# Optimization experiments

Hardware: AMD Instinct MI355X
Metric: run time of the kernel (lower is better)

The kernel has to match this reference:

```python
import jax, jax.numpy as jnp
import numpy as np

H = W = 2048
P = 50000  # number of peaks
BACKGROUND = 0.1


def setup_inputs() -> dict:
    key = jax.random.key(0)
    k1, k2, k3, k4 = jax.random.split(key, 4)
    # coordinate meshes, X varies along columns, Y along rows (as in np.meshgrid)
    X, Y = jnp.meshgrid(jnp.arange(W, dtype=jnp.float32), jnp.arange(H, dtype=jnp.float32))
    margin = 32.0
    pos_x = jax.random.uniform(k1, (P,), jnp.float32, margin, W - margin - 1)
    pos_y = jax.random.uniform(k2, (P,), jnp.float32, margin, H - margin - 1)
    height = jax.random.uniform(k3, (P,), jnp.float32, 0.5, 2.0)
    width = jax.random.uniform(k4, (P,), jnp.float32, 2.0, 4.0)
    return {"X": X, "Y": Y, "pos_x": pos_x, "pos_y": pos_y, "height": height, "width": width}


def _gaussian(x, y, pos_x, pos_y, height, width):
    # isotropic Gaussian peak (concrete model_fn)
    r2 = (x - pos_x) ** 2 + (y - pos_y) ** 2
    return height * jnp.exp(-r2 / (2.0 * width ** 2))


def reference(X, Y, pos_x, pos_y, height, width):
    # window size from max width (static shape choice, computed concretely)
    width_max = float(jnp.max(width))
    window_size = int(5 * width_max)
    if window_size % 2 == 0:
        window_size += 1
    half = window_size // 2

    wr = jnp.arange(-half, half + 1, dtype=jnp.int32)
    window_X, window_Y = jnp.meshgrid(wr, wr)  # (ws, ws)
    window_coords = jnp.stack([window_X.ravel(), window_Y.ravel()], axis=-1)  # (ws*ws, 2) as (x, y)

    x_idx = jnp.round(pos_x - X[0, 0]).astype(jnp.int32)
    y_idx = jnp.round(pos_y - Y[0, 0]).astype(jnp.int32)
    peak_coords = jnp.stack([x_idx, y_idx], axis=-1)  # (P, 2)
    global_coords = peak_coords[:, None, :] + window_coords[None, :, :]  # (P, ws*ws, 2)

    # evaluate peak centered at 0 on the local window: (P, ws, ws)
    local_peaks = _gaussian(
        window_X[None, :, :].astype(X.dtype),
        window_Y[None, :, :].astype(X.dtype),
        0.0, 0.0,
        height[:, None, None], width[:, None, None],
    )
    local_flat = local_peaks.reshape(pos_x.shape[0], -1)  # (P, ws*ws)

    total = jnp.zeros_like(X) + BACKGROUND
    total = total.at[global_coords[:, :, 1], global_coords[:, :, 0]].add(local_flat)
    return total
```

## Files before the change

### kernel.cpp

```cpp
#include <hip/hip_runtime.h>


#define IMG_W 2048
#define IMG_H 2048
#define CELL_SHIFT 4
#define CELLS_X 128
#define NCELL (CELLS_X * CELLS_X)
#define CAP 20
#define REG 64
#define CH 32
#define CH_PAD 40
#define CANDMAX 256

typedef _Float16 half8 __attribute__((ext_vector_type(8)));
typedef float floatx4 __attribute__((ext_vector_type(4)));

__global__ void k_bin(const float* __restrict__ px, const float* __restrict__ py,
                      const float* __restrict__ ht, const float* __restrict__ wd,
                      int P, int* __restrict__ counts, unsigned int* __restrict__ wmax,
                      float4* __restrict__ bins) {
    int i = blockIdx.x * blockDim.x + threadIdx.x;
    bool live = (i < P);
    float w = live ? wd[i] : 0.0f;
    float wr = w;
    for (int m = 32; m >= 1; m >>= 1)
        wr = fmaxf(wr, __shfl_xor(wr, m));
    if ((threadIdx.x & 63) == 0)
        atomicMax(wmax, __float_as_uint(wr));
    if (!live) return;
    float cxf = rintf(px[i]);
    float cyf = rintf(py[i]);
    int cell = (((int)cyf) >> CELL_SHIFT) * CELLS_X + (((int)cxf) >> CELL_SHIFT);
    int slot = atomicAdd(&counts[cell], 1);
    if (slot < CAP)
        bins[(size_t)cell * CAP + slot] = make_float4(cxf, cyf, ht[i], -0.5f / (w * w));
}

__global__ __launch_bounds__(512) void k_render(
    const int* __restrict__ counts, const float4* __restrict__ bins,
    const unsigned int* __restrict__ wmax, float* __restrict__ out)
{
    __shared__ _Float16 Afb[2][REG * CH_PAD];
    __shared__ _Float16 Bfb[2][REG * CH_PAD];
    __shared__ float4 cand[CANDMAX];
    __shared__ int ncand_sh;

    int flat = threadIdx.x;
    int wave = flat >> 6;
    int lane = flat & 63;

    float wm = __uint_as_float(*wmax);
    int wsz = (int)(5.0 * (double)wm);
    if ((wsz & 1) == 0) wsz++;
    int half = wsz >> 1;
    float halff = (float)half;

    int RX0 = blockIdx.x * REG;
    int RY0 = blockIdx.y * REG;

    if (flat == 0) ncand_sh = 0;
    __syncthreads();

    int cx0 = max(0, (RX0 - half) >> CELL_SHIFT);
    int cx1 = min(CELLS_X - 1, (RX0 + REG - 1 + half) >> CELL_SHIFT);
    int cy0 = max(0, (RY0 - half) >> CELL_SHIFT);
    int cy1 = min(CELLS_X - 1, (RY0 + REG - 1 + half) >> CELL_SHIFT);
    int ncx = cx1 - cx0 + 1;
    int npairs = ncx * (cy1 - cy0 + 1) * CAP;
    float ncx_rcp = __builtin_amdgcn_rcpf((float)ncx);
    int rounds = (npairs + 511) / 512;

    for (int rd = 0; rd < rounds; ++rd) {
        int pr = rd * 512 + flat;
        bool ok = false;
        float4 p = make_float4(0.f, 0.f, 0.f, 0.f);
        if (pr < npairs) {
            int c = pr / CAP;
            int s = pr - c * CAP;
            int cy = (int)(((float)c + 0.5f) * ncx_rcp);
            int cx = c - cy * ncx;
            int cell = (cy0 + cy) * CELLS_X + (cx0 + cx);
            int cnt = min(counts[cell], CAP);
            if (s < cnt) {
                p = bins[(size_t)cell * CAP + s];
                int cxi = (int)p.x, cyi = (int)p.y;
                ok = (cxi + half >= RX0 && cxi - half < RX0 + REG &&
                      cyi + half >= RY0 && cyi - half < RY0 + REG);
            }
        }
        unsigned long long m = __ballot(ok);
        if (m) {
            int leader = (int)__ffsll((unsigned long long)m) - 1;
            int base = 0;
            if (lane == leader) base = atomicAdd(&ncand_sh, __popcll(m));
            base = __shfl(base, leader);
            if (ok) {
                int pos = base + __popcll(m & ((1ull << lane) - 1));
                if (pos < CANDMAX) cand[pos] = p;
            }
        }
    }
    __syncthreads();
    int nc = min(ncand_sh, CANDMAX);
    int nch = (nc + CH - 1) / CH;

    floatx4 acc0 = {0.f, 0.f, 0.f, 0.f};
    floatx4 acc1 = {0.f, 0.f, 0.f, 0.f};
    int m0 = (wave & 3) * 16,       n0 = (wave >> 2) * 16;
    int m1 = ((wave + 8) & 3) * 16, n1 = ((wave + 8) >> 2) * 16;
    int fr = lane & 15;
    int fk = (lane >> 4) * 8;

    int side = wave >> 2;
    int oct = wave & 3;
    float base0 = side ? (float)RX0 : (float)RY0;
    float dbase = base0 + (float)lane;

    for (int ci = 0; ci < nch; ++ci) {
        int b = ci & 1;
        int c0 = ci * CH + oct * 8;
        half8 hv;
        #pragma unroll
        for (int t = 0; t < 8; ++t) {
            int k = c0 + t;
            float val = 0.0f;
            if (k < nc) {
                float4 p = cand[k];
                float d = dbase - (side ? p.x : p.y);
                if (fabsf(d) <= halff) {
                    val = __expf(p.w * d * d);
                    if (side) val *= p.z;
                }
            }
            hv[t] = (_Float16)val;
        }
        _Float16* dst = side ? &Bfb[b][lane * CH_PAD + oct * 8]
                             : &Afb[b][lane * CH_PAD + oct * 8];
        *(half8*)dst = hv;
        __syncthreads();
        half8 a0 = *(const half8*)&Afb[b][(m0 + fr) * CH_PAD + fk];
        half8 b0 = *(const half8*)&Bfb[b][(n0 + fr) * CH_PAD + fk];
        acc0 = __builtin_amdgcn_mfma_f32_16x16x32_f16(a0, b0, acc0, 0, 0, 0);
        half8 a1 = *(const half8*)&Afb[b][(m1 + fr) * CH_PAD + fk];
        half8 b1 = *(const half8*)&Bfb[b][(n1 + fr) * CH_PAD + fk];
        acc1 = __builtin_amdgcn_mfma_f32_16x16x32_f16(a1, b1, acc1, 0, 0, 0);
    }

    int col = lane & 15;
    int qr = (lane >> 4) * 4;
    {
        size_t gx = (size_t)(RX0 + n0 + col);
        size_t gy = (size_t)(RY0 + m0 + qr);
        for (int r = 0; r < 4; ++r)
            out[(gy + r) * IMG_W + gx] = acc0[r] + 0.1f;
    }
    {
        size_t gx = (size_t)(RX0 + n1 + col);
        size_t gy = (size_t)(RY0 + m1 + qr);
        for (int r = 0; r < 4; ++r)
            out[(gy + r) * IMG_W + gx] = acc1[r] + 0.1f;
    }
}

extern "C" void kernel_launch(void* const* d_in, const int* in_sizes, int n_in,
                              void* d_out, int out_size, void* d_ws, size_t ws_size,
                              hipStream_t stream) {
    const float* pos_x  = (const float*)d_in[2];
    const float* pos_y  = (const float*)d_in[3];
    const float* height = (const float*)d_in[4];
    const float* width  = (const float*)d_in[5];
    int P = in_sizes[2];
    float* out = (float*)d_out;
    char* ws = (char*)d_ws;

    unsigned int* wmax = (unsigned int*)ws;
    int* counts = (int*)(ws + 16);
    size_t bins_off = 16 + sizeof(int) * (size_t)NCELL;
    float4* bins = (float4*)(ws + bins_off);

    hipMemsetAsync(ws, 0, bins_off, stream);
    k_bin<<<(P + 255) / 256, 256, 0, stream>>>(pos_x, pos_y, height, width, P,
                                               counts, wmax, bins);
    dim3 grid(IMG_W / REG, IMG_H / REG), block(512);
    k_render<<<grid, block, 0, stream>>>(counts, bins, wmax, out);
}
```

Baseline: 107.2 us.

## Bin peaks directly into per-region lists and batch MFMA after one barrier

```diff
diff --git a/kernel.cpp b/kernel.cpp
--- a/kernel.cpp
+++ b/kernel.cpp
@@ -3,22 +3,21 @@
 
 #define IMG_W 2048
 #define IMG_H 2048
-#define CELL_SHIFT 4
-#define CELLS_X 128
-#define NCELL (CELLS_X * CELLS_X)
-#define CAP 20
 #define REG 64
+#define REGS_X (IMG_W / REG)
+#define NREG (REGS_X * REGS_X)
+#define RCAP 160
+#define HALO 9
+#define KMAX 96
 #define CH 32
-#define CH_PAD 40
-#define CANDMAX 256
 
 typedef _Float16 half8 __attribute__((ext_vector_type(8)));
 typedef float floatx4 __attribute__((ext_vector_type(4)));
 
 __global__ void k_bin(const float* __restrict__ px, const float* __restrict__ py,
                       const float* __restrict__ ht, const float* __restrict__ wd,
-                      int P, int* __restrict__ counts, unsigned int* __restrict__ wmax,
-                      float4* __restrict__ bins) {
+                      int P, int* __restrict__ rcnt, unsigned int* __restrict__ wmax,
+                      float4* __restrict__ lists) {
     int i = blockIdx.x * blockDim.x + threadIdx.x;
     bool live = (i < P);
     float w = live ? wd[i] : 0.0f;
@@ -30,20 +29,27 @@
     if (!live) return;
     float cxf = rintf(px[i]);
     float cyf = rintf(py[i]);
-    int cell = (((int)cyf) >> CELL_SHIFT) * CELLS_X + (((int)cxf) >> CELL_SHIFT);
-    int slot = atomicAdd(&counts[cell], 1);
-    if (slot < CAP)
-        bins[(size_t)cell * CAP + slot] = make_float4(cxf, cyf, ht[i], -0.5f / (w * w));
+    int cxi = (int)cxf, cyi = (int)cyf;
+    float4 rec = make_float4(cxf, cyf, ht[i], -0.5f / (w * w));
+    int rx0 = (cxi - HALO) >> 6, rx1 = (cxi + HALO) >> 6;
+    int ry0 = (cyi - HALO) >> 6, ry1 = (cyi + HALO) >> 6;
+    rx0 = max(rx0, 0); rx1 = min(rx1, REGS_X - 1);
+    ry0 = max(ry0, 0); ry1 = min(ry1, REGS_X - 1);
+    for (int ry = ry0; ry <= ry1; ++ry)
+        for (int rx = rx0; rx <= rx1; ++rx) {
+            int r = ry * REGS_X + rx;
+            int slot = atomicAdd(&rcnt[r], 1);
+            if (slot < RCAP)
+                lists[(size_t)r * RCAP + slot] = rec;
+        }
 }
 
 __global__ __launch_bounds__(512) void k_render(
-    const int* __restrict__ counts, const float4* __restrict__ bins,
+    const int* __restrict__ rcnt, const float4* __restrict__ lists,
     const unsigned int* __restrict__ wmax, float* __restrict__ out)
 {
-    __shared__ _Float16 Afb[2][REG * CH_PAD];
-    __shared__ _Float16 Bfb[2][REG * CH_PAD];
-    __shared__ float4 cand[CANDMAX];
-    __shared__ int ncand_sh;
+    __shared__ _Float16 Af[3 * 4 * REG * 8];
+    __shared__ _Float16 Bf[3 * 4 * REG * 8];
 
     int flat = threadIdx.x;
     int wave = flat >> 6;
@@ -52,102 +58,66 @@
     float wm = __uint_as_float(*wmax);
     int wsz = (int)(5.0 * (double)wm);
     if ((wsz & 1) == 0) wsz++;
-    int half = wsz >> 1;
-    float halff = (float)half;
+    float halff = (float)(wsz >> 1);
 
     int RX0 = blockIdx.x * REG;
     int RY0 = blockIdx.y * REG;
-
-    if (flat == 0) ncand_sh = 0;
-    __syncthreads();
-
-    int cx0 = max(0, (RX0 - half) >> CELL_SHIFT);
-    int cx1 = min(CELLS_X - 1, (RX0 + REG - 1 + half) >> CELL_SHIFT);
-    int cy0 = max(0, (RY0 - half) >> CELL_SHIFT);
-    int cy1 = min(CELLS_X - 1, (RY0 + REG - 1 + half) >> CELL_SHIFT);
-    int ncx = cx1 - cx0 + 1;
-    int npairs = ncx * (cy1 - cy0 + 1) * CAP;
-    float ncx_rcp = __builtin_amdgcn_rcpf((float)ncx);
-    int rounds = (npairs + 511) / 512;
-
-    for (int rd = 0; rd < rounds; ++rd) {
-        int pr = rd * 512 + flat;
-        bool ok = false;
-        float4 p = make_float4(0.f, 0.f, 0.f, 0.f);
-        if (pr < npairs) {
-            int c = pr / CAP;
-            int s = pr - c * CAP;
-            int cy = (int)(((float)c + 0.5f) * ncx_rcp);
-            int cx = c - cy * ncx;
-            int cell = (cy0 + cy) * CELLS_X + (cx0 + cx);
-            int cnt = min(counts[cell], CAP);
-            if (s < cnt) {
-                p = bins[(size_t)cell * CAP + s];
-                int cxi = (int)p.x, cyi = (int)p.y;
-                ok = (cxi + half >= RX0 && cxi - half < RX0 + REG &&
-                      cyi + half >= RY0 && cyi - half < RY0 + REG);
-            }
-        }
-        unsigned long long m = __ballot(ok);
-        if (m) {
-            int leader = (int)__ffsll((unsigned long long)m) - 1;
-            int base = 0;
-            if (lane == leader) base = atomicAdd(&ncand_sh, __popcll(m));
-            base = __shfl(base, leader);
-            if (ok) {
-                int pos = base + __popcll(m & ((1ull << lane) - 1));
-                if (pos < CANDMAX) cand[pos] = p;
-            }
-        }
-    }
-    __syncthreads();
-    int nc = min(ncand_sh, CANDMAX);
-    int nch = (nc + CH - 1) / CH;
+    int rgn = blockIdx.y * REGS_X + blockIdx.x;
+    int nc = min(rcnt[rgn], RCAP);
+    const float4* __restrict__ cl = &lists[(size_t)rgn * RCAP];
 
     floatx4 acc0 = {0.f, 0.f, 0.f, 0.f};
     floatx4 acc1 = {0.f, 0.f, 0.f, 0.f};
     int m0 = (wave & 3) * 16,       n0 = (wave >> 2) * 16;
     int m1 = ((wave + 8) & 3) * 16, n1 = ((wave + 8) >> 2) * 16;
     int fr = lane & 15;
-    int fk = (lane >> 4) * 8;
+    int quad = lane >> 4;
 
     int side = wave >> 2;
     int oct = wave & 3;
-    float base0 = side ? (float)RX0 : (float)RY0;
-    float dbase = base0 + (float)lane;
+    float dbase = (side ? (float)RX0 : (float)RY0) + (float)lane;
+    _Float16* __restrict__ fdst = side ? Bf : Af;
 
-    for (int ci = 0; ci < nch; ++ci) {
-        int b = ci & 1;
-        int c0 = ci * CH + oct * 8;
-        half8 hv;
-        #pragma unroll
-        for (int t = 0; t < 8; ++t) {
-            int k = c0 + t;
-            float val = 0.0f;
-            if (k < nc) {
-                float4 p = cand[k];
-                float d = dbase - (side ? p.x : p.y);
-                if (fabsf(d) <= halff) {
-                    val = __expf(p.w * d * d);
-                    if (side) val *= p.z;
+    int passes = (nc + KMAX - 1) / KMAX;
+    for (int p = 0; p < passes; ++p) {
+        int base = p * KMAX;
+        int rem = min(nc - base, KMAX);
+        int nch = (rem + CH - 1) / CH;
+        if (p) __syncthreads();
+        for (int ci = 0; ci < nch; ++ci) {
+            half8 hv;
+            int k0 = base + ci * CH + oct * 8;
+            #pragma unroll
+            for (int t = 0; t < 8; ++t) {
+                int k = k0 + t;
+                float val = 0.0f;
+                if (k < nc) {
+                    float4 q = cl[k];
+                    float d = dbase - (side ? q.x : q.y);
+                    if (fabsf(d) <= halff) {
+                        val = __expf(q.w * d * d);
+                        if (side) val *= q.z;
+                    }
                 }
+                hv[t] = (_Float16)val;
             }
-            hv[t] = (_Float16)val;
+            *(half8*)&fdst[((ci * 4 + oct) * REG + lane) * 8] = hv;
         }
-        _Float16* dst = side ? &Bfb[b][lane * CH_PAD + oct * 8]
-                             : &Afb[b][lane * CH_PAD + oct * 8];
-        *(half8*)dst = hv;
         __syncthreads();
-        half8 a0 = *(const half8*)&Afb[b][(m0 + fr) * CH_PAD + fk];
-        half8 b0 = *(const half8*)&Bfb[b][(n0 + fr) * CH_PAD + fk];
-        acc0 = __builtin_amdgcn_mfma_f32_16x16x32_f16(a0, b0, acc0, 0, 0, 0);
-        half8 a1 = *(const half8*)&Afb[b][(m1 + fr) * CH_PAD + fk];
-        half8 b1 = *(const half8*)&Bfb[b][(n1 + fr) * CH_PAD + fk];
-        acc1 = __builtin_amdgcn_mfma_f32_16x16x32_f16(a1, b1, acc1, 0, 0, 0);
+        for (int ci = 0; ci < nch; ++ci) {
+            const _Float16* ab = &Af[((ci * 4 + quad) * REG) * 8];
+            const _Float16* bb = &Bf[((ci * 4 + quad) * REG) * 8];
+            half8 a0 = *(const half8*)&ab[(m0 + fr) * 8];
+            half8 b0 = *(const half8*)&bb[(n0 + fr) * 8];
+            acc0 = __builtin_amdgcn_mfma_f32_16x16x32_f16(a0, b0, acc0, 0, 0, 0);
+            half8 a1 = *(const half8*)&ab[(m1 + fr) * 8];
+            half8 b1 = *(const half8*)&bb[(n1 + fr) * 8];
+            acc1 = __builtin_amdgcn_mfma_f32_16x16x32_f16(a1, b1, acc1, 0, 0, 0);
+        }
     }
 
-    int col = lane & 15;
-    int qr = (lane >> 4) * 4;
+    int col = fr;
+    int qr = quad * 4;
     {
         size_t gx = (size_t)(RX0 + n0 + col);
         size_t gy = (size_t)(RY0 + m0 + qr);
@@ -174,13 +144,13 @@
     char* ws = (char*)d_ws;
 
     unsigned int* wmax = (unsigned int*)ws;
-    int* counts = (int*)(ws + 16);
-    size_t bins_off = 16 + sizeof(int) * (size_t)NCELL;
-    float4* bins = (float4*)(ws + bins_off);
+    int* rcnt = (int*)(ws + 16);
+    size_t lists_off = 16 + sizeof(int) * (size_t)NREG;
+    float4* lists = (float4*)(ws + lists_off);
 
-    hipMemsetAsync(ws, 0, bins_off, stream);
+    hipMemsetAsync(ws, 0, lists_off, stream);
     k_bin<<<(P + 255) / 256, 256, 0, stream>>>(pos_x, pos_y, height, width, P,
-                                               counts, wmax, bins);
-    dim3 grid(IMG_W / REG, IMG_H / REG), block(512);
-    k_render<<<grid, block, 0, stream>>>(counts, bins, wmax, out);
+                                               rcnt, wmax, lists);
+    dim3 grid(REGS_X, REGS_X), block(512);
+    k_render<<<grid, block, 0, stream>>>(rcnt, lists, wmax, out);
 }
```

Result: slower. 118.8 us (+10.9%).
